# Kernel tuning notes

Hardware: AMD Instinct MI355X
Metric: run time of the kernel (lower is better)

## Reference

```python
import jax, jax.numpy as jnp
import numpy as np


def setup_inputs() -> dict:
    key = jax.random.key(0)
    k1, k2, k3 = jax.random.split(key, 3)
    inp = jax.random.normal(k1, (32, 128, 56, 56), dtype=jnp.float32)
    # kaiming-style scale for a 3x3 conv kernel
    fan_in = 128 * 3 * 3
    kernel = jax.random.normal(k2, (256, 128, 3, 3), dtype=jnp.float32) * np.float32(np.sqrt(2.0 / fan_in))
    bias = jax.random.normal(k3, (256,), dtype=jnp.float32)
    return {"inp": inp, "kernel": kernel, "bias": bias}


def reference(inp, kernel, bias):
    # 3x3 conv, stride 1, padding 1 (SAME), NCHW / OIHW layout, plus bias.
    out = jax.lax.conv_general_dilated(
        inp, kernel,
        window_strides=(1, 1),
        padding=((1, 1), (1, 1)),
        dimension_numbers=("NCHW", "OIHW", "NCHW"),
    )
    return out + bias[None, :, None, None]
```

## Files before the change

### kernel.cpp

```cpp
#include <hip/hip_runtime.h>
#include <hip/hip_bf16.h>


#define C_IN   128
#define K_OUT  256
#define HW     56
#define IMG    3136
#define NBATCH 32
#define PW     58
#define IN_WS_USHORT ((size_t)4*NBATCH*PW*256*8)
#define WT_WS_USHORT ((size_t)12*2*1536*8)

typedef __bf16 bf16x8 __attribute__((ext_vector_type(8)));
typedef float  f32x4  __attribute__((ext_vector_type(4)));
typedef unsigned short ushort8 __attribute__((ext_vector_type(8)));

__device__ inline unsigned short f2bf(float f) {
    unsigned int u = __builtin_bit_cast(unsigned int, f);
    u += ((u >> 16) & 1u) + 0x7FFFu;
    return (unsigned short)(u >> 16);
}

__device__ __forceinline__ void gl2lds16(const unsigned short* g, unsigned short* l) {
    __builtin_amdgcn_global_load_lds(
        (const __attribute__((address_space(1))) unsigned int*)g,
        (__attribute__((address_space(3))) unsigned int*)l, 16, 0, 0);
}

__global__ void prep_input(const float* __restrict__ inp,
                           unsigned short* __restrict__ dst) {
    __shared__ unsigned short tile[C_IN * 57];
    int n = blockIdx.x / PW, py = blockIdx.x % PW;
    ushort8* d8 = (ushort8*)dst;
    const bool border = (py == 0 || py == PW - 1);
    if (!border) {
        const float* src = inp + (size_t)n * C_IN * IMG + (py - 1) * HW;
        for (int i = threadIdx.x; i < C_IN * HW; i += 256) {
            int c = i / HW, x = i - c * HW;
            tile[c * 57 + x] = f2bf(src[c * IMG + x]);
        }
        __syncthreads();
    }
    for (int i = threadIdx.x; i < 1024; i += 256) {
        int cq = i >> 8, rem = i & 255;
        int X = ((rem >> 6) & 3) * 16 + (rem & 15);
        int cc = (rem >> 4) & 3;
        ushort8 v = (ushort8)0;
        if (!border && X >= 1 && X <= HW) {
#pragma unroll
            for (int e = 0; e < 8; ++e)
                v[e] = tile[(cq * 32 + cc * 8 + e) * 57 + (X - 1)];
        }
        d8[((size_t)(cq * NBATCH + n) * PW + py) * 256 + rem] = v;
    }
}

__global__ void prep_weights(const float* __restrict__ w,
                             unsigned short* __restrict__ dst) {
    int chunk = blockIdx.x * 256 + threadIdx.x;
    int p = chunk / 3072, rem = chunk - p * 3072;
    int koh = rem / 1536, rem2 = rem - koh * 1536;
    int s = rem2 / 512, rem3 = rem2 - s * 512;
    int koq = rem3 >> 6, cc = (rem3 >> 4) & 3, kor = rem3 & 15;
    int ko = koh * 128 + koq * 16 + kor;
    int cq = p / 3, r = p - 3 * cq;
    ushort8 v;
#pragma unroll
    for (int e = 0; e < 8; ++e)
        v[e] = f2bf(w[(ko * C_IN + cq * 32 + cc * 8 + e) * 9 + r * 3 + s]);
    ((ushort8*)dst)[chunk] = v;
}

__global__ __launch_bounds__(128, 2) void conv_mfma(
        const unsigned short* __restrict__ In,
        const unsigned short* __restrict__ Wt,
        const float* __restrict__ bias,
        float* __restrict__ out) {
    __shared__ unsigned short smem[16384];

    const int tid = threadIdx.x;
    const int lane = tid & 63, wv = tid >> 6;
    const int l15 = lane & 15, lk = lane >> 4;
    const int koh = blockIdx.y;
    const int by = blockIdx.x;
    const int n = by / 28, rb = (by % 28) * 2;

    const int wlane = wv * 2048 + lk * 128 + l15 * 8;

    int yl[7], xp[3][7];
#pragma unroll
    for (int nf = 0; nf < 7; ++nf) {
        int p = nf * 16 + l15;
        yl[nf] = p / 56;
        int x = p - yl[nf] * 56;
#pragma unroll
        for (int s = 0; s < 3; ++s) {
            int X = x + s;
            xp[s][nf] = ((X >> 4) << 10) + lk * 256 + ((X & 15) << 4);
        }
    }

    f32x4 acc[4][7];
#pragma unroll
    for (int m = 0; m < 4; ++m)
#pragma unroll
        for (int nf = 0; nf < 7; ++nf) acc[m][nf] = (f32x4)0.0f;

    bf16x8 wbuf[2][4];

#define LOAD_WS(G_) do {                                                    \
    if constexpr ((G_) <= 35) {                                             \
        constexpr int p_ = (G_) / 3, sx_ = (G_) % 3;                        \
        const unsigned short* wp = Wt + ((size_t)(p_ * 2 + koh)) * 12288    \
                                   + sx_ * 4096 + wlane;                    \
        _Pragma("unroll")                                                   \
        for (int m = 0; m < 4; ++m)                                         \
            wbuf[(G_) & 1][m] = *(const bf16x8*)(wp + m * 512);             \
    } } while (0)

#define STAGE_ROW(C_, T_) do {                                              \
    const unsigned short* gsrc =                                            \
        In + ((size_t)(((C_) * NBATCH + n) * PW + rb + (T_))) * 2048;       \
    unsigned short* ldst = &smem[((4 * (C_) + (T_)) & 7) * 2048];           \
    gl2lds16(gsrc + tid * 8, ldst + tid * 8);                               \
    gl2lds16(gsrc + 1024 + tid * 8, ldst + 1024 + tid * 8);                 \
} while (0)

#define STEP(PH, S_) do {                                                   \
    constexpr int g_ = (PH) * 3 + (S_);                                     \
    LOAD_WS(g_ + 1);                                                        \
    { const char* ib = (const char*)smem;                                   \
      bf16x8 b[7];                                                          \
      _Pragma("unroll")                                                     \
      for (int nf = 0; nf < 7; ++nf)                                        \
          b[nf] = *(const bf16x8*)(ib + roff[nf] + xp[(S_)][nf]);           \
      __builtin_amdgcn_s_setprio(1);                                        \
      _Pragma("unroll")                                                     \
      for (int m = 0; m < 4; ++m)                                           \
          _Pragma("unroll")                                                 \
          for (int nf = 0; nf < 7; ++nf)                                    \
              acc[m][nf] = __builtin_amdgcn_mfma_f32_16x16x32_bf16(         \
                  wbuf[g_ & 1][m], b[nf], acc[m][nf], 0, 0, 0);             \
      __builtin_amdgcn_s_setprio(0);                                        \
    }                                                                       \
} while (0)

    STAGE_ROW(0, 0); STAGE_ROW(0, 1); STAGE_ROW(0, 2); STAGE_ROW(0, 3);
    asm volatile("" ::: "memory");
    LOAD_WS(0);

#define PHASE(PH) do {                                                      \
    constexpr int cqp_ = (PH) / 3, rp_ = (PH) % 3;                          \
    asm volatile("s_waitcnt vmcnt(4)" ::: "memory");                        \
    asm volatile("s_barrier" ::: "memory");                                 \
    if constexpr (cqp_ < 3) {                                               \
        if constexpr (rp_ == 0) { STAGE_ROW(cqp_ + 1, 0); STAGE_ROW(cqp_ + 1, 1); } \
        if constexpr (rp_ == 1) { STAGE_ROW(cqp_ + 1, 2); STAGE_ROW(cqp_ + 1, 3); } \
        if constexpr (rp_ != 2) asm volatile("" ::: "memory");              \
    }                                                                       \
    { int roff[7];                                                          \
      _Pragma("unroll")                                                     \
      for (int nf = 0; nf < 7; ++nf)                                        \
          roff[nf] = ((4 * cqp_ + rp_ + yl[nf]) & 7) << 12;                 \
      STEP(PH, 0); STEP(PH, 1); STEP(PH, 2);                                \
    }                                                                       \
} while (0)

    PHASE(0);  PHASE(1);  PHASE(2);  PHASE(3);
    PHASE(4);  PHASE(5);  PHASE(6);  PHASE(7);
    PHASE(8);  PHASE(9);  PHASE(10); PHASE(11);

#undef PHASE
#undef STEP
#undef STAGE_ROW
#undef LOAD_WS

    const int sp0 = rb * 56;
#pragma unroll
    for (int m = 0; m < 4; ++m) {
        int kb = koh * 128 + wv * 64 + m * 16 + lk * 4;
        f32x4 bs = *(const f32x4*)(bias + kb);
#pragma unroll
        for (int nf = 0; nf < 7; ++nf) {
            float* ob = out + ((size_t)(n * K_OUT + kb) * IMG) + sp0 + nf * 16 + l15;
#pragma unroll
            for (int j = 0; j < 4; ++j)
                ob[(size_t)j * IMG] = acc[m][nf][j] + bs[j];
        }
    }
}

__global__ void conv_naive(const float* __restrict__ inp,
                           const float* __restrict__ ker,
                           const float* __restrict__ bias,
                           float* __restrict__ out, int total) {
    int o = blockIdx.x * blockDim.x + threadIdx.x;
    if (o >= total) return;
    int x = o % HW, y = (o / HW) % HW, ko = (o / IMG) % K_OUT, n = o / (IMG * K_OUT);
    float acc = bias[ko];
    for (int c = 0; c < C_IN; ++c)
        for (int r = 0; r < 3; ++r) {
            int iy = y + r - 1; if ((unsigned)iy >= HW) continue;
            for (int s = 0; s < 3; ++s) {
                int ix = x + s - 1; if ((unsigned)ix >= HW) continue;
                acc += inp[((n * C_IN + c) * HW + iy) * HW + ix]
                     * ker[((ko * C_IN + c) * 3 + r) * 3 + s];
            }
        }
    out[o] = acc;
}

extern "C" void kernel_launch(void* const* d_in, const int* in_sizes, int n_in,
                              void* d_out, int out_size, void* d_ws, size_t ws_size,
                              hipStream_t stream) {
    const float* inp  = (const float*)d_in[0];
    const float* ker  = (const float*)d_in[1];
    const float* bias = (const float*)d_in[2];
    float* out = (float*)d_out;

    const size_t need = (IN_WS_USHORT + WT_WS_USHORT) * 2;
    if (ws_size < need) {
        int total = NBATCH * K_OUT * IMG;
        conv_naive<<<(total + 255) / 256, 256, 0, stream>>>(inp, ker, bias, out, total);
        return;
    }

    unsigned short* inb = (unsigned short*)d_ws;
    unsigned short* wtb = inb + IN_WS_USHORT;

    prep_input<<<NBATCH * PW, 256, 0, stream>>>(inp, inb);
    prep_weights<<<144, 256, 0, stream>>>(ker, wtb);

    conv_mfma<<<dim3(896, 2), 128, 0, stream>>>(inb, wtb, bias, out);
}
```

Baseline: 82.51 us.

## Stage conv weights through double-buffered LDS instead of per-wave register loads

Weights that each wave previously loaded straight from global memory into a register double buffer are now copied into a double-buffered LDS region with global_load_lds, one phase ahead. The MFMA steps read their A operands from LDS alongside the input rows. This is meant to remove the global-load latency on the weight path and the redundant per-wave fetches. In exchange, LDS use rises from 32 KB to 80 KB per block, which can lower occupancy, and the wait becomes a full vmcnt(0) every phase.

```diff
diff --git a/kernel.cpp b/kernel.cpp
--- a/kernel.cpp
+++ b/kernel.cpp
@@ -76,7 +76,7 @@
         const unsigned short* __restrict__ Wt,
         const float* __restrict__ bias,
         float* __restrict__ out) {
-    __shared__ unsigned short smem[16384];
+    __shared__ unsigned short smem[40960];
 
     const int tid = threadIdx.x;
     const int lane = tid & 63, wv = tid >> 6;
@@ -85,7 +85,7 @@
     const int by = blockIdx.x;
     const int n = by / 28, rb = (by % 28) * 2;
 
-    const int wlane = wv * 2048 + lk * 128 + l15 * 8;
+    const int abase = wv * 4096 + lk * 256 + l15 * 16;
 
     int yl[7], xp[3][7];
 #pragma unroll
@@ -106,58 +106,55 @@
 #pragma unroll
         for (int nf = 0; nf < 7; ++nf) acc[m][nf] = (f32x4)0.0f;
 
-    bf16x8 wbuf[2][4];
-
-#define LOAD_WS(G_) do {                                                    \
-    if constexpr ((G_) <= 35) {                                             \
-        constexpr int p_ = (G_) / 3, sx_ = (G_) % 3;                        \
-        const unsigned short* wp = Wt + ((size_t)(p_ * 2 + koh)) * 12288    \
-                                   + sx_ * 4096 + wlane;                    \
-        _Pragma("unroll")                                                   \
-        for (int m = 0; m < 4; ++m)                                         \
-            wbuf[(G_) & 1][m] = *(const bf16x8*)(wp + m * 512);             \
-    } } while (0)
+#define STAGE_W(P_) do {                                                    \
+    const unsigned short* wg = Wt + ((size_t)((P_) * 2 + koh)) * 12288;     \
+    unsigned short* wl = &smem[((P_) & 1) * 12288];                         \
+    _Pragma("unroll")                                                       \
+    for (int i = 0; i < 12; ++i)                                            \
+        gl2lds16(wg + i * 1024 + tid * 8, wl + i * 1024 + tid * 8);         \
+} while (0)
 
 #define STAGE_ROW(C_, T_) do {                                              \
     const unsigned short* gsrc =                                            \
         In + ((size_t)(((C_) * NBATCH + n) * PW + rb + (T_))) * 2048;       \
-    unsigned short* ldst = &smem[((4 * (C_) + (T_)) & 7) * 2048];           \
+    unsigned short* ldst = &smem[24576 + ((4 * (C_) + (T_)) & 7) * 2048];   \
     gl2lds16(gsrc + tid * 8, ldst + tid * 8);                               \
     gl2lds16(gsrc + 1024 + tid * 8, ldst + 1024 + tid * 8);                 \
 } while (0)
 
 #define STEP(PH, S_) do {                                                   \
-    constexpr int g_ = (PH) * 3 + (S_);                                     \
-    LOAD_WS(g_ + 1);                                                        \
-    { const char* ib = (const char*)smem;                                   \
-      bf16x8 b[7];                                                          \
-      _Pragma("unroll")                                                     \
-      for (int nf = 0; nf < 7; ++nf)                                        \
-          b[nf] = *(const bf16x8*)(ib + roff[nf] + xp[(S_)][nf]);           \
-      __builtin_amdgcn_s_setprio(1);                                        \
-      _Pragma("unroll")                                                     \
-      for (int m = 0; m < 4; ++m)                                           \
-          _Pragma("unroll")                                                 \
-          for (int nf = 0; nf < 7; ++nf)                                    \
-              acc[m][nf] = __builtin_amdgcn_mfma_f32_16x16x32_bf16(         \
-                  wbuf[g_ & 1][m], b[nf], acc[m][nf], 0, 0, 0);             \
-      __builtin_amdgcn_s_setprio(0);                                        \
-    }                                                                       \
-} while (0)
-
+    const char* wb = (const char*)smem + ((PH) & 1) * 24576 + (S_) * 8192;  \
+    const char* ib = (const char*)smem + 49152;                             \
+    bf16x8 a[4], b[7];                                                      \
+    _Pragma("unroll")                                                       \
+    for (int m = 0; m < 4; ++m)                                             \
+        a[m] = *(const bf16x8*)(wb + abase + m * 1024);                     \
+    _Pragma("unroll")                                                       \
+    for (int nf = 0; nf < 7; ++nf)                                          \
+        b[nf] = *(const bf16x8*)(ib + roff[nf] + xp[(S_)][nf]);             \
+    __builtin_amdgcn_s_setprio(1);                                          \
+    _Pragma("unroll")                                                       \
+    for (int m = 0; m < 4; ++m)                                             \
+        _Pragma("unroll")                                                   \
+        for (int nf = 0; nf < 7; ++nf)                                      \
+            acc[m][nf] = __builtin_amdgcn_mfma_f32_16x16x32_bf16(           \
+                a[m], b[nf], acc[m][nf], 0, 0, 0);                          \
+    __builtin_amdgcn_s_setprio(0);                                          \
+} while (0)
+
+    STAGE_W(0);
     STAGE_ROW(0, 0); STAGE_ROW(0, 1); STAGE_ROW(0, 2); STAGE_ROW(0, 3);
-    asm volatile("" ::: "memory");
-    LOAD_WS(0);
 
 #define PHASE(PH) do {                                                      \
     constexpr int cqp_ = (PH) / 3, rp_ = (PH) % 3;                          \
-    asm volatile("s_waitcnt vmcnt(4)" ::: "memory");                        \
+    asm volatile("s_waitcnt vmcnt(0)" ::: "memory");                        \
     asm volatile("s_barrier" ::: "memory");                                 \
+    if constexpr ((PH) < 11) STAGE_W((PH) + 1);                             \
     if constexpr (cqp_ < 3) {                                               \
         if constexpr (rp_ == 0) { STAGE_ROW(cqp_ + 1, 0); STAGE_ROW(cqp_ + 1, 1); } \
         if constexpr (rp_ == 1) { STAGE_ROW(cqp_ + 1, 2); STAGE_ROW(cqp_ + 1, 3); } \
-        if constexpr (rp_ != 2) asm volatile("" ::: "memory");              \
     }                                                                       \
+    asm volatile("" ::: "memory");                                          \
     { int roff[7];                                                          \
       _Pragma("unroll")                                                     \
       for (int nf = 0; nf < 7; ++nf)                                        \
@@ -173,7 +170,7 @@
 #undef PHASE
 #undef STEP
 #undef STAGE_ROW
-#undef LOAD_WS
+#undef STAGE_W
 
     const int sp0 = rb * 56;
 #pragma unroll
```

New measurement: 93.90 us. +13.8%, slower.
